# Optimization experiments

Measured on AMD Instinct MI355X. Metric: run time of the kernel, lower is better.

## Reference

```python
import jax, jax.numpy as jnp
import numpy as np

BETA = 1.0
EPS = 1e-12  # F.normalize eps

def _normalize(x):
    # F.normalize(x, dim=1): x shape (B, N, 1)
    n = jnp.sqrt(jnp.sum(x * x, axis=1, keepdims=True))
    return x / jnp.maximum(n, EPS)

def _step(M, x):
    return _normalize(jnp.matmul(M, x))

def _eigval(M, x):
    # x^T M x / ||x||^2, x: (B, N, 1)
    Mx = jnp.matmul(M, x)                          # (B, N, 1)
    num = jnp.sum(Mx * x, axis=(1, 2))             # (B,)
    den = jnp.sum(x * x, axis=(1, 2))              # (B,)
    return num / den

def setup_inputs() -> dict:
    key = jax.random.key(0)
    kA, kx = jax.random.split(key)
    A = jax.random.normal(kA, (64, 512, 28, 28), dtype=jnp.float32)
    x0 = jax.random.normal(kx, (64, 512, 1), dtype=jnp.float32)
    return {"A": A, "x0": x0}

def reference(A, x0):
    B, C, H, W = A.shape
    Wm = A.reshape(B, C, H * W)                    # (B, C, HW)
    AAT = jnp.einsum('bcd,bed->bce', Wm, Wm)       # (B, C, C)

    # --- dominant_eigenvalue(AAT): first call initializes last_x (no grad, 3 iters) ---
    xi = _normalize(x0)
    for _ in range(3):
        xi = _step(AAT, xi)
    xi = jax.lax.stop_gradient(xi)                 # last_x after no-grad init
    x1 = _step(AAT, xi)                            # 1 differentiable iter
    largest = _eigval(AAT, x1)                     # (B,)
    last_x = jax.lax.stop_gradient(x1)             # self.last_x = x.detach()

    # --- dominant_eigenvalue(AAT - largest*I): reuses last_x, 1 iter ---
    I = jnp.eye(C, dtype=A.dtype)[None]            # (1, C, C)
    A2 = AAT - largest[:, None, None] * I
    x2 = _step(A2, last_x)
    tmp = _eigval(A2, x2)

    smallest = tmp + largest
    penalty = BETA * (largest / smallest - 1.0) ** 2
    return jnp.sum(penalty) / B
```

## Files before the change

### kernel.cpp

```cpp
#include <hip/hip_runtime.h>
#include <math.h>


#define BB 64
#define CC 512
#define DD 784
#define DCH 16
#define NSPLIT 7
#define NCHPS 7
#define F4PR 196
#define BF4 100352
#define FEPS 1e-12f

__device__ __forceinline__ void gload16(const float4* gp, float4* lp) {
    __builtin_amdgcn_global_load_lds(
        (const __attribute__((address_space(1))) void*)gp,
        (__attribute__((address_space(3))) void*)lp, 16, 0, 0);
}

__device__ __forceinline__ float blk_reduce(float s, float* red) {
    for (int off = 32; off; off >>= 1) s += __shfl_down(s, off, 64);
    int w = threadIdx.x >> 6;
    if ((threadIdx.x & 63) == 0) red[w] = s;
    __syncthreads();
    float t = red[0] + red[1] + red[2] + red[3];
    __syncthreads();
    return t;
}

__global__ __launch_bounds__(256, 3)
void k_repack(const float* __restrict__ A, float* __restrict__ T) {
    __shared__ float4 lds4[16 * F4PR];
    const int tid = threadIdx.x, lane = tid & 63, w = tid >> 6;
    const int b = blockIdx.y, c0 = blockIdx.x * 16;
    const float4* src4 = (const float4*)A + ((size_t)b * CC + c0) * F4PR;
#pragma unroll
    for (int i = 0; i < 12; i++)
        gload16(src4 + i * 256 + w * 64 + lane, lds4 + i * 256 + w * 64);
    if (w == 0) gload16(src4 + 3072 + lane, lds4 + 3072);
    __syncthreads();
    float4* dst4 = (float4*)T + (size_t)b * BF4;
#pragma unroll
    for (int j = 0; j < 13; j++) {
        int idx = j * 256 + tid;
        if (idx < 3136) {
            int chq = idx >> 4, i = idx & 15;
            dst4[(size_t)chq * CC + c0 + i] = lds4[i * F4PR + chq];
        }
    }
}

template <bool RP>
__global__ __launch_bounds__(256, 2)
void k_step(const float* __restrict__ M, const float* __restrict__ xin,
            const int nparts, float* __restrict__ vout) {
    __shared__ float xs[CC];
    __shared__ float vws[4][CC];
    __shared__ float red[4];

    const int tid = threadIdx.x;
    const int b = blockIdx.y, s = blockIdx.x;
    const int lane = tid & 63, w = tid >> 6;
    const float4* Mb = (const float4*)M + (size_t)b * BF4;

    const float* xp = xin + (size_t)b * nparts * CC;
    float xv0 = 0.f, xv1 = 0.f;
    for (int p = 0; p < nparts; p++) {
        xv0 += xp[p * CC + tid];
        xv1 += xp[p * CC + tid + 256];
    }
    float ss = blk_reduce(xv0 * xv0 + xv1 * xv1, red);
    float rn = 1.0f / fmaxf(sqrtf(ss), FEPS);
    xs[tid] = xv0 * rn;
    xs[tid + 256] = xv1 * rn;
    __syncthreads();

    float xk[8];
#pragma unroll
    for (int k = 0; k < 8; k++) xk[k] = xs[lane + 64 * k];

    const int ch0 = s * NCHPS;
    float4 a[2][8];
    float vk[8] = {0.f, 0.f, 0.f, 0.f, 0.f, 0.f, 0.f, 0.f};

    auto load = [&](int ch, float4* dst) {
        if (RP) {
            const float4* g = Mb + (size_t)(ch * 4 + w) * CC + lane;
#pragma unroll
            for (int k = 0; k < 8; k++) dst[k] = g[64 * k];
        } else {
            const float4* g = Mb + (size_t)lane * F4PR + ch * 4 + w;
#pragma unroll
            for (int k = 0; k < 8; k++) dst[k] = g[(size_t)64 * k * F4PR];
        }
    };

    load(ch0, a[0]);
#pragma unroll
    for (int j = 0; j < NCHPS; j++) {
        const int cb = j & 1;
        if (j + 1 < NCHPS) load(ch0 + j + 1, a[cb ^ 1]);

        float4 ua = make_float4(0.f, 0.f, 0.f, 0.f);
#pragma unroll
        for (int k = 0; k < 8; k++) {
            ua.x += a[cb][k].x * xk[k]; ua.y += a[cb][k].y * xk[k];
            ua.z += a[cb][k].z * xk[k]; ua.w += a[cb][k].w * xk[k];
        }
#pragma unroll
        for (int off = 1; off < 64; off <<= 1) {
            ua.x += __shfl_xor(ua.x, off, 64);
            ua.y += __shfl_xor(ua.y, off, 64);
            ua.z += __shfl_xor(ua.z, off, 64);
            ua.w += __shfl_xor(ua.w, off, 64);
        }

#pragma unroll
        for (int k = 0; k < 8; k++)
            vk[k] += a[cb][k].x * ua.x + a[cb][k].y * ua.y +
                     a[cb][k].z * ua.z + a[cb][k].w * ua.w;
    }

#pragma unroll
    for (int k = 0; k < 8; k++) vws[w][lane + 64 * k] = vk[k];
    __syncthreads();
    float* vp = vout + ((size_t)b * NSPLIT + s) * CC;
    vp[tid]       = vws[0][tid] + vws[1][tid] + vws[2][tid] + vws[3][tid];
    vp[tid + 256] = vws[0][tid + 256] + vws[1][tid + 256] +
                    vws[2][tid + 256] + vws[3][tid + 256];
}

__global__ void k_mid(const float* __restrict__ t4, const float* __restrict__ t5,
                      float* __restrict__ acc, float* __restrict__ y) {
    __shared__ float red[4];
    int b = blockIdx.x;
    const float* p4 = t4 + (size_t)b * NSPLIT * CC;
    const float* p5 = t5 + (size_t)b * NSPLIT * CC;
    float a0 = 0.f, a1 = 0.f, b0 = 0.f, b1 = 0.f;
    for (int p = 0; p < NSPLIT; p++) {
        a0 += p4[p * CC + threadIdx.x]; a1 += p4[p * CC + threadIdx.x + 256];
        b0 += p5[p * CC + threadIdx.x]; b1 += p5[p * CC + threadIdx.x + 256];
    }
    float ss4 = blk_reduce(a0 * a0 + a1 * a1, red);
    float rn = 1.0f / fmaxf(sqrtf(ss4), FEPS);
    float x10 = a0 * rn, x11 = a1 * rn;
    float num = blk_reduce(b0 * x10 + b1 * x11, red);
    float den = blk_reduce(x10 * x10 + x11 * x11, red);
    float largest = num / den;
    float* yp = y + (size_t)b * CC;
    yp[threadIdx.x] = b0 - largest * x10;
    yp[threadIdx.x + 256] = b1 - largest * x11;
    if (threadIdx.x == 0) acc[b * 8 + 0] = largest;
}

__global__ void k_fin2(const float* __restrict__ w, const float* __restrict__ y,
                       float* __restrict__ acc) {
    __shared__ float red[4];
    int b = blockIdx.x;
    const float* wp = w + (size_t)b * NSPLIT * CC;
    const float* yp = y + (size_t)b * CC;
    float w0 = 0.f, w1 = 0.f;
    for (int p = 0; p < NSPLIT; p++) {
        w0 += wp[p * CC + threadIdx.x];
        w1 += wp[p * CC + threadIdx.x + 256];
    }
    float y0 = yp[threadIdx.x], y1 = yp[threadIdx.x + 256];
    float ssy = blk_reduce(y0 * y0 + y1 * y1, red);
    float rn = 1.0f / fmaxf(sqrtf(ssy), FEPS);
    float x20 = y0 * rn, x21 = y1 * rn;
    float dotwx = blk_reduce(w0 * x20 + w1 * x21, red);
    float den2 = blk_reduce(x20 * x20 + x21 * x21, red);
    if (threadIdx.x == 0) { acc[b * 8 + 1] = dotwx; acc[b * 8 + 2] = den2; }
}

__global__ void k_out(const float* __restrict__ acc, float* __restrict__ out) {
    int b = threadIdx.x;
    float largest = acc[b * 8 + 0];
    float dotwx   = acc[b * 8 + 1];
    float den2    = acc[b * 8 + 2];
    float tmp = (dotwx - largest * den2) / den2;
    float smallest = tmp + largest;
    float r = largest / smallest - 1.0f;
    float pen = r * r;
    for (int off = 32; off; off >>= 1) pen += __shfl_down(pen, off, 64);
    if (b == 0) out[0] = pen / (float)BB;
}

extern "C" void kernel_launch(void* const* d_in, const int* in_sizes, int n_in,
                              void* d_out, int out_size, void* d_ws, size_t ws_size,
                              hipStream_t stream) {
    const float* A  = (const float*)d_in[0];
    const float* x0 = (const float*)d_in[1];
    float* out = (float*)d_out;
    float* ws = (float*)d_ws;

    float* acc = ws;
    float* y   = ws + 512;
    float* PA  = y + BB * CC;
    float* PB  = PA + BB * NSPLIT * CC;
    float* T   = PB + BB * NSPLIT * CC;
    const size_t need = ((size_t)492032 + (size_t)BB * BF4 * 4) * sizeof(float);

    dim3 gS(NSPLIT, BB);
    if (ws_size >= need) {
        k_repack<<<dim3(32, BB), 256, 0, stream>>>(A, T);
        k_step<true><<<gS, 256, 0, stream>>>(T, x0, 1, PA);
        k_step<true><<<gS, 256, 0, stream>>>(T, PA, NSPLIT, PB);
        k_step<true><<<gS, 256, 0, stream>>>(T, PB, NSPLIT, PA);
        k_step<true><<<gS, 256, 0, stream>>>(T, PA, NSPLIT, PB);
        k_step<true><<<gS, 256, 0, stream>>>(T, PB, NSPLIT, PA);
        k_mid<<<BB, 256, 0, stream>>>(PB, PA, acc, y);
        k_step<true><<<gS, 256, 0, stream>>>(T, y, 1, PB);
        k_fin2<<<BB, 256, 0, stream>>>(PB, y, acc);
    } else {
        k_step<false><<<gS, 256, 0, stream>>>(A, x0, 1, PA);
        k_step<false><<<gS, 256, 0, stream>>>(A, PA, NSPLIT, PB);
        k_step<false><<<gS, 256, 0, stream>>>(A, PB, NSPLIT, PA);
        k_step<false><<<gS, 256, 0, stream>>>(A, PA, NSPLIT, PB);
        k_step<false><<<gS, 256, 0, stream>>>(A, PB, NSPLIT, PA);
        k_mid<<<BB, 256, 0, stream>>>(PB, PA, acc, y);
        k_step<false><<<gS, 256, 0, stream>>>(A, y, 1, PB);
        k_fin2<<<BB, 256, 0, stream>>>(PB, y, acc);
    }
    k_out<<<1, 64, 0, stream>>>(acc, out);
}
```

Baseline: 274.2 us.

## Split matvec into one chunk per block and hoist normalization into separate kernel

The step kernel now gives each block a single 4-float4 chunk of the d dimension (49 splits instead of 7 with double-buffered loops). Input normalization moves out of every step block into a small per-batch k_norm kernel, so blocks no longer each redo the partial-sum reduction. The repack kernel uses 8-row tiles with higher occupancy. This raises parallelism and occupancy but adds several extra kernel launches and larger partial buffers (49 partials per batch) to reduce.

```diff
diff --git a/kernel.cpp b/kernel.cpp
--- a/kernel.cpp
+++ b/kernel.cpp
@@ -5,9 +5,8 @@
 #define BB 64
 #define CC 512
 #define DD 784
-#define DCH 16
-#define NSPLIT 7
-#define NCHPS 7
+#define NCH 49
+#define QTOT 196
 #define F4PR 196
 #define BF4 100352
 #define FEPS 1e-12f
@@ -28,142 +27,140 @@
     return t;
 }
 
-__global__ __launch_bounds__(256, 3)
+__global__ __launch_bounds__(256, 6)
 void k_repack(const float* __restrict__ A, float* __restrict__ T) {
-    __shared__ float4 lds4[16 * F4PR];
+    __shared__ float4 lds4[8 * F4PR];
     const int tid = threadIdx.x, lane = tid & 63, w = tid >> 6;
-    const int b = blockIdx.y, c0 = blockIdx.x * 16;
-    const float4* src4 = (const float4*)A + ((size_t)b * CC + c0) * F4PR;
-#pragma unroll
-    for (int i = 0; i < 12; i++)
+    const int b = blockIdx.y, R0 = blockIdx.x * 8;
+    const float4* src4 = (const float4*)A + ((size_t)b * CC + R0) * F4PR;
+#pragma unroll
+    for (int i = 0; i < 6; i++)
         gload16(src4 + i * 256 + w * 64 + lane, lds4 + i * 256 + w * 64);
-    if (w == 0) gload16(src4 + 3072 + lane, lds4 + 3072);
+    if (w == 0 && lane < 32) gload16(src4 + 1536 + lane, lds4 + 1536);
     __syncthreads();
     float4* dst4 = (float4*)T + (size_t)b * BF4;
 #pragma unroll
-    for (int j = 0; j < 13; j++) {
+    for (int j = 0; j < 7; j++) {
         int idx = j * 256 + tid;
-        if (idx < 3136) {
-            int chq = idx >> 4, i = idx & 15;
-            dst4[(size_t)chq * CC + c0 + i] = lds4[i * F4PR + chq];
+        if (idx < 8 * F4PR) {
+            int chq = idx >> 3, i = idx & 7;
+            dst4[(size_t)chq * CC + R0 + i] = lds4[i * F4PR + chq];
         }
     }
 }
 
+__global__ void k_norm(const float* __restrict__ in, const int nparts,
+                       float* __restrict__ out) {
+    __shared__ float red[4];
+    int b = blockIdx.x;
+    const float* ip = in + (size_t)b * nparts * CC;
+    float v0 = 0.f, v1 = 0.f;
+    for (int p = 0; p < nparts; p++) {
+        v0 += ip[p * CC + threadIdx.x];
+        v1 += ip[p * CC + threadIdx.x + 256];
+    }
+    float ss = blk_reduce(v0 * v0 + v1 * v1, red);
+    float rn = 1.0f / fmaxf(sqrtf(ss), FEPS);
+    float* op = out + (size_t)b * CC;
+    op[threadIdx.x] = v0 * rn;
+    op[threadIdx.x + 256] = v1 * rn;
+}
+
 template <bool RP>
-__global__ __launch_bounds__(256, 2)
-void k_step(const float* __restrict__ M, const float* __restrict__ xin,
-            const int nparts, float* __restrict__ vout) {
+__global__ __launch_bounds__(256, 4)
+void k_step(const float* __restrict__ M, const float* __restrict__ xhat,
+            float* __restrict__ vout) {
     __shared__ float xs[CC];
     __shared__ float vws[4][CC];
-    __shared__ float red[4];
 
     const int tid = threadIdx.x;
     const int b = blockIdx.y, s = blockIdx.x;
     const int lane = tid & 63, w = tid >> 6;
+    const int chq = s * 4 + w;
     const float4* Mb = (const float4*)M + (size_t)b * BF4;
 
-    const float* xp = xin + (size_t)b * nparts * CC;
-    float xv0 = 0.f, xv1 = 0.f;
-    for (int p = 0; p < nparts; p++) {
-        xv0 += xp[p * CC + tid];
-        xv1 += xp[p * CC + tid + 256];
-    }
-    float ss = blk_reduce(xv0 * xv0 + xv1 * xv1, red);
-    float rn = 1.0f / fmaxf(sqrtf(ss), FEPS);
-    xs[tid] = xv0 * rn;
-    xs[tid + 256] = xv1 * rn;
-    __syncthreads();
-
+    float4 a[8];
+    if (RP) {
+        const float4* g = Mb + (size_t)chq * CC + lane;
+#pragma unroll
+        for (int k = 0; k < 8; k++) a[k] = g[64 * k];
+    } else {
+        const float4* g = Mb + (size_t)lane * F4PR + chq;
+#pragma unroll
+        for (int k = 0; k < 8; k++) a[k] = g[(size_t)64 * k * F4PR];
+    }
+
+    const float* xp = xhat + (size_t)b * CC;
+    xs[tid] = xp[tid];
+    xs[tid + 256] = xp[tid + 256];
+    __syncthreads();
     float xk[8];
 #pragma unroll
     for (int k = 0; k < 8; k++) xk[k] = xs[lane + 64 * k];
 
-    const int ch0 = s * NCHPS;
-    float4 a[2][8];
-    float vk[8] = {0.f, 0.f, 0.f, 0.f, 0.f, 0.f, 0.f, 0.f};
-
-    auto load = [&](int ch, float4* dst) {
-        if (RP) {
-            const float4* g = Mb + (size_t)(ch * 4 + w) * CC + lane;
-#pragma unroll
-            for (int k = 0; k < 8; k++) dst[k] = g[64 * k];
-        } else {
-            const float4* g = Mb + (size_t)lane * F4PR + ch * 4 + w;
-#pragma unroll
-            for (int k = 0; k < 8; k++) dst[k] = g[(size_t)64 * k * F4PR];
-        }
-    };
-
-    load(ch0, a[0]);
-#pragma unroll
-    for (int j = 0; j < NCHPS; j++) {
-        const int cb = j & 1;
-        if (j + 1 < NCHPS) load(ch0 + j + 1, a[cb ^ 1]);
-
-        float4 ua = make_float4(0.f, 0.f, 0.f, 0.f);
-#pragma unroll
-        for (int k = 0; k < 8; k++) {
-            ua.x += a[cb][k].x * xk[k]; ua.y += a[cb][k].y * xk[k];
-            ua.z += a[cb][k].z * xk[k]; ua.w += a[cb][k].w * xk[k];
-        }
-#pragma unroll
-        for (int off = 1; off < 64; off <<= 1) {
-            ua.x += __shfl_xor(ua.x, off, 64);
-            ua.y += __shfl_xor(ua.y, off, 64);
-            ua.z += __shfl_xor(ua.z, off, 64);
-            ua.w += __shfl_xor(ua.w, off, 64);
-        }
-
-#pragma unroll
-        for (int k = 0; k < 8; k++)
-            vk[k] += a[cb][k].x * ua.x + a[cb][k].y * ua.y +
-                     a[cb][k].z * ua.z + a[cb][k].w * ua.w;
-    }
+    float4 ua = make_float4(0.f, 0.f, 0.f, 0.f);
+#pragma unroll
+    for (int k = 0; k < 8; k++) {
+        ua.x += a[k].x * xk[k]; ua.y += a[k].y * xk[k];
+        ua.z += a[k].z * xk[k]; ua.w += a[k].w * xk[k];
+    }
+#pragma unroll
+    for (int off = 1; off < 64; off <<= 1) {
+        ua.x += __shfl_xor(ua.x, off, 64);
+        ua.y += __shfl_xor(ua.y, off, 64);
+        ua.z += __shfl_xor(ua.z, off, 64);
+        ua.w += __shfl_xor(ua.w, off, 64);
+    }
+
+    float vk[8];
+#pragma unroll
+    for (int k = 0; k < 8; k++)
+        vk[k] = a[k].x * ua.x + a[k].y * ua.y + a[k].z * ua.z + a[k].w * ua.w;
 
 #pragma unroll
     for (int k = 0; k < 8; k++) vws[w][lane + 64 * k] = vk[k];
     __syncthreads();
-    float* vp = vout + ((size_t)b * NSPLIT + s) * CC;
+    float* vp = vout + ((size_t)b * NCH + s) * CC;
     vp[tid]       = vws[0][tid] + vws[1][tid] + vws[2][tid] + vws[3][tid];
     vp[tid + 256] = vws[0][tid + 256] + vws[1][tid + 256] +
                     vws[2][tid + 256] + vws[3][tid + 256];
 }
 
-__global__ void k_mid(const float* __restrict__ t4, const float* __restrict__ t5,
-                      float* __restrict__ acc, float* __restrict__ y) {
+__global__ void k_mid(const float* __restrict__ x1, const float* __restrict__ P,
+                      float* __restrict__ acc, float* __restrict__ yhat) {
     __shared__ float red[4];
     int b = blockIdx.x;
-    const float* p4 = t4 + (size_t)b * NSPLIT * CC;
-    const float* p5 = t5 + (size_t)b * NSPLIT * CC;
-    float a0 = 0.f, a1 = 0.f, b0 = 0.f, b1 = 0.f;
-    for (int p = 0; p < NSPLIT; p++) {
-        a0 += p4[p * CC + threadIdx.x]; a1 += p4[p * CC + threadIdx.x + 256];
-        b0 += p5[p * CC + threadIdx.x]; b1 += p5[p * CC + threadIdx.x + 256];
-    }
-    float ss4 = blk_reduce(a0 * a0 + a1 * a1, red);
-    float rn = 1.0f / fmaxf(sqrtf(ss4), FEPS);
-    float x10 = a0 * rn, x11 = a1 * rn;
-    float num = blk_reduce(b0 * x10 + b1 * x11, red);
+    const float* pp = P + (size_t)b * NCH * CC;
+    float m0 = 0.f, m1 = 0.f;
+    for (int p = 0; p < NCH; p++) {
+        m0 += pp[p * CC + threadIdx.x];
+        m1 += pp[p * CC + threadIdx.x + 256];
+    }
+    const float* xp = x1 + (size_t)b * CC;
+    float x10 = xp[threadIdx.x], x11 = xp[threadIdx.x + 256];
+    float num = blk_reduce(m0 * x10 + m1 * x11, red);
     float den = blk_reduce(x10 * x10 + x11 * x11, red);
     float largest = num / den;
-    float* yp = y + (size_t)b * CC;
-    yp[threadIdx.x] = b0 - largest * x10;
-    yp[threadIdx.x + 256] = b1 - largest * x11;
+    float y0 = m0 - largest * x10, y1 = m1 - largest * x11;
+    float ssy = blk_reduce(y0 * y0 + y1 * y1, red);
+    float rn = 1.0f / fmaxf(sqrtf(ssy), FEPS);
+    float* yp = yhat + (size_t)b * CC;
+    yp[threadIdx.x] = y0 * rn;
+    yp[threadIdx.x + 256] = y1 * rn;
     if (threadIdx.x == 0) acc[b * 8 + 0] = largest;
 }
 
-__global__ void k_fin2(const float* __restrict__ w, const float* __restrict__ y,
+__global__ void k_fin2(const float* __restrict__ P, const float* __restrict__ yhat,
                        float* __restrict__ acc) {
     __shared__ float red[4];
     int b = blockIdx.x;
-    const float* wp = w + (size_t)b * NSPLIT * CC;
-    const float* yp = y + (size_t)b * CC;
+    const float* pp = P + (size_t)b * NCH * CC;
     float w0 = 0.f, w1 = 0.f;
-    for (int p = 0; p < NSPLIT; p++) {
-        w0 += wp[p * CC + threadIdx.x];
-        w1 += wp[p * CC + threadIdx.x + 256];
-    }
+    for (int p = 0; p < NCH; p++) {
+        w0 += pp[p * CC + threadIdx.x];
+        w1 += pp[p * CC + threadIdx.x + 256];
+    }
+    const float* yp = yhat + (size_t)b * CC;
     float y0 = yp[threadIdx.x], y1 = yp[threadIdx.x + 256];
     float ssy = blk_reduce(y0 * y0 + y1 * y1, red);
     float rn = 1.0f / fmaxf(sqrtf(ssy), FEPS);
@@ -195,32 +192,44 @@
     float* ws = (float*)d_ws;
 
     float* acc = ws;
-    float* y   = ws + 512;
-    float* PA  = y + BB * CC;
-    float* PB  = PA + BB * NSPLIT * CC;
-    float* T   = PB + BB * NSPLIT * CC;
-    const size_t need = ((size_t)492032 + (size_t)BB * BF4 * 4) * sizeof(float);
-
-    dim3 gS(NSPLIT, BB);
+    float* X   = ws + 512;
+    float* Y   = X + BB * CC;
+    float* P   = Y + BB * CC;
+    float* T   = P + (size_t)BB * NCH * CC;
+    const size_t need =
+        ((size_t)512 + 2 * BB * CC + (size_t)BB * NCH * CC +
+         (size_t)BB * CC * DD) * sizeof(float);
+
+    dim3 gS(NCH, BB);
     if (ws_size >= need) {
-        k_repack<<<dim3(32, BB), 256, 0, stream>>>(A, T);
-        k_step<true><<<gS, 256, 0, stream>>>(T, x0, 1, PA);
-        k_step<true><<<gS, 256, 0, stream>>>(T, PA, NSPLIT, PB);
-        k_step<true><<<gS, 256, 0, stream>>>(T, PB, NSPLIT, PA);
-        k_step<true><<<gS, 256, 0, stream>>>(T, PA, NSPLIT, PB);
-        k_step<true><<<gS, 256, 0, stream>>>(T, PB, NSPLIT, PA);
-        k_mid<<<BB, 256, 0, stream>>>(PB, PA, acc, y);
-        k_step<true><<<gS, 256, 0, stream>>>(T, y, 1, PB);
-        k_fin2<<<BB, 256, 0, stream>>>(PB, y, acc);
+        k_repack<<<dim3(CC / 8, BB), 256, 0, stream>>>(A, T);
+        k_norm<<<BB, 256, 0, stream>>>(x0, 1, X);
+        k_step<true><<<gS, 256, 0, stream>>>(T, X, P);
+        k_norm<<<BB, 256, 0, stream>>>(P, NCH, X);
+        k_step<true><<<gS, 256, 0, stream>>>(T, X, P);
+        k_norm<<<BB, 256, 0, stream>>>(P, NCH, X);
+        k_step<true><<<gS, 256, 0, stream>>>(T, X, P);
+        k_norm<<<BB, 256, 0, stream>>>(P, NCH, X);
+        k_step<true><<<gS, 256, 0, stream>>>(T, X, P);
+        k_norm<<<BB, 256, 0, stream>>>(P, NCH, X);
+        k_step<true><<<gS, 256, 0, stream>>>(T, X, P);
+        k_mid<<<BB, 256, 0, stream>>>(X, P, acc, Y);
+        k_step<true><<<gS, 256, 0, stream>>>(T, Y, P);
+        k_fin2<<<BB, 256, 0, stream>>>(P, Y, acc);
     } else {
-        k_step<false><<<gS, 256, 0, stream>>>(A, x0, 1, PA);
-        k_step<false><<<gS, 256, 0, stream>>>(A, PA, NSPLIT, PB);
-        k_step<false><<<gS, 256, 0, stream>>>(A, PB, NSPLIT, PA);
-        k_step<false><<<gS, 256, 0, stream>>>(A, PA, NSPLIT, PB);
-        k_step<false><<<gS, 256, 0, stream>>>(A, PB, NSPLIT, PA);
-        k_mid<<<BB, 256, 0, stream>>>(PB, PA, acc, y);
-        k_step<false><<<gS, 256, 0, stream>>>(A, y, 1, PB);
-        k_fin2<<<BB, 256, 0, stream>>>(PB, y, acc);
+        k_norm<<<BB, 256, 0, stream>>>(x0, 1, X);
+        k_step<false><<<gS, 256, 0, stream>>>(A, X, P);
+        k_norm<<<BB, 256, 0, stream>>>(P, NCH, X);
+        k_step<false><<<gS, 256, 0, stream>>>(A, X, P);
+        k_norm<<<BB, 256, 0, stream>>>(P, NCH, X);
+        k_step<false><<<gS, 256, 0, stream>>>(A, X, P);
+        k_norm<<<BB, 256, 0, stream>>>(P, NCH, X);
+        k_step<false><<<gS, 256, 0, stream>>>(A, X, P);
+        k_norm<<<BB, 256, 0, stream>>>(P, NCH, X);
+        k_step<false><<<gS, 256, 0, stream>>>(A, X, P);
+        k_mid<<<BB, 256, 0, stream>>>(X, P, acc, Y);
+        k_step<false><<<gS, 256, 0, stream>>>(A, Y, P);
+        k_fin2<<<BB, 256, 0, stream>>>(P, Y, acc);
     }
     k_out<<<1, 64, 0, stream>>>(acc, out);
 }
```

Result: slower. 332.0 us (+21.1%).

## Retile repack layout into 64-row blocks and split step kernel 16-way with prefetch

Applied to the files above, without the earlier changes.

The repacked matrix layout changes to 64-channel row blocks, so each wave's float4 loads cover a contiguous 1KB segment. Repack now uses XOR-swizzled LDS transposes over 64x28 tiles instead of global_load_lds. The step kernel splits work into 16 parts with interleaved quads and more blocks per CU. It issues the first two matrix loads before the x-normalisation reduction to hide latency. The cost is more partial sums for downstream kernels to reduce and uneven work, since some waves get 3 quads and others 4.

```diff
diff --git a/kernel.cpp b/kernel.cpp
--- a/kernel.cpp
+++ b/kernel.cpp
@@ -5,18 +5,13 @@
 #define BB 64
 #define CC 512
 #define DD 784
-#define DCH 16
-#define NSPLIT 7
-#define NCHPS 7
+#define NSPLIT 16
+#define NQ 196
 #define F4PR 196
 #define BF4 100352
+#define QT 28
+#define CBS 12544
 #define FEPS 1e-12f
-
-__device__ __forceinline__ void gload16(const float4* gp, float4* lp) {
-    __builtin_amdgcn_global_load_lds(
-        (const __attribute__((address_space(1))) void*)gp,
-        (__attribute__((address_space(3))) void*)lp, 16, 0, 0);
-}
 
 __device__ __forceinline__ float blk_reduce(float s, float* red) {
     for (int off = 32; off; off >>= 1) s += __shfl_down(s, off, 64);
@@ -28,30 +23,36 @@
     return t;
 }
 
-__global__ __launch_bounds__(256, 3)
+__global__ __launch_bounds__(256, 5)
 void k_repack(const float* __restrict__ A, float* __restrict__ T) {
-    __shared__ float4 lds4[16 * F4PR];
-    const int tid = threadIdx.x, lane = tid & 63, w = tid >> 6;
-    const int b = blockIdx.y, c0 = blockIdx.x * 16;
-    const float4* src4 = (const float4*)A + ((size_t)b * CC + c0) * F4PR;
-#pragma unroll
-    for (int i = 0; i < 12; i++)
-        gload16(src4 + i * 256 + w * 64 + lane, lds4 + i * 256 + w * 64);
-    if (w == 0) gload16(src4 + 3072 + lane, lds4 + 3072);
-    __syncthreads();
-    float4* dst4 = (float4*)T + (size_t)b * BF4;
-#pragma unroll
-    for (int j = 0; j < 13; j++) {
+    __shared__ float4 lds4[64 * QT];
+    const int tid = threadIdx.x;
+    const int b = blockIdx.y, tile = blockIdx.x;
+    const int cb = tile / 7, qt = tile % 7;
+    const int R0 = cb * 64, q0 = qt * QT;
+    const int r = tid >> 2, qg = tid & 3;
+    const float4* src = (const float4*)A +
+        ((size_t)b * CC + R0 + r) * F4PR + q0 + qg * 7;
+    float4 a[7];
+#pragma unroll
+    for (int j = 0; j < 7; j++) a[j] = src[j];
+    const int xr = (r >> 2) & 3;
+#pragma unroll
+    for (int j = 0; j < 7; j++)
+        lds4[r * QT + ((qg * 7 + j) ^ xr)] = a[j];
+    __syncthreads();
+    float4* dst = (float4*)T + (size_t)b * BF4 + (size_t)cb * CBS +
+                  (size_t)q0 * 64;
+#pragma unroll
+    for (int j = 0; j < 7; j++) {
         int idx = j * 256 + tid;
-        if (idx < 3136) {
-            int chq = idx >> 4, i = idx & 15;
-            dst4[(size_t)chq * CC + c0 + i] = lds4[i * F4PR + chq];
-        }
+        int chq = idx >> 6, i = idx & 63;
+        dst[idx] = lds4[i * QT + (chq ^ ((i >> 2) & 3))];
     }
 }
 
 template <bool RP>
-__global__ __launch_bounds__(256, 2)
+__global__ __launch_bounds__(256, 4)
 void k_step(const float* __restrict__ M, const float* __restrict__ xin,
             const int nparts, float* __restrict__ vout) {
     __shared__ float xs[CC];
@@ -61,51 +62,29 @@
     const int tid = threadIdx.x;
     const int b = blockIdx.y, s = blockIdx.x;
     const int lane = tid & 63, w = tid >> 6;
+    const int q0 = s * 4 + w;
     const float4* Mb = (const float4*)M + (size_t)b * BF4;
 
-    const float* xp = xin + (size_t)b * nparts * CC;
-    float xv0 = 0.f, xv1 = 0.f;
-    for (int p = 0; p < nparts; p++) {
-        xv0 += xp[p * CC + tid];
-        xv1 += xp[p * CC + tid + 256];
-    }
-    float ss = blk_reduce(xv0 * xv0 + xv1 * xv1, red);
-    float rn = 1.0f / fmaxf(sqrtf(ss), FEPS);
-    xs[tid] = xv0 * rn;
-    xs[tid + 256] = xv1 * rn;
-    __syncthreads();
-
     float xk[8];
-#pragma unroll
-    for (int k = 0; k < 8; k++) xk[k] = xs[lane + 64 * k];
-
-    const int ch0 = s * NCHPS;
-    float4 a[2][8];
     float vk[8] = {0.f, 0.f, 0.f, 0.f, 0.f, 0.f, 0.f, 0.f};
 
-    auto load = [&](int ch, float4* dst) {
+    auto loadq = [&](int q, float4* d) {
         if (RP) {
-            const float4* g = Mb + (size_t)(ch * 4 + w) * CC + lane;
-#pragma unroll
-            for (int k = 0; k < 8; k++) dst[k] = g[64 * k];
+            const float4* g = Mb + (size_t)q * 64 + lane;
+#pragma unroll
+            for (int k = 0; k < 8; k++) d[k] = g[(size_t)k * CBS];
         } else {
-            const float4* g = Mb + (size_t)lane * F4PR + ch * 4 + w;
-#pragma unroll
-            for (int k = 0; k < 8; k++) dst[k] = g[(size_t)64 * k * F4PR];
+            const float4* g = Mb + (size_t)lane * F4PR + q;
+#pragma unroll
+            for (int k = 0; k < 8; k++) d[k] = g[(size_t)64 * k * F4PR];
         }
     };
-
-    load(ch0, a[0]);
-#pragma unroll
-    for (int j = 0; j < NCHPS; j++) {
-        const int cb = j & 1;
-        if (j + 1 < NCHPS) load(ch0 + j + 1, a[cb ^ 1]);
-
+    auto computeq = [&](const float4* a) {
         float4 ua = make_float4(0.f, 0.f, 0.f, 0.f);
 #pragma unroll
         for (int k = 0; k < 8; k++) {
-            ua.x += a[cb][k].x * xk[k]; ua.y += a[cb][k].y * xk[k];
-            ua.z += a[cb][k].z * xk[k]; ua.w += a[cb][k].w * xk[k];
+            ua.x += a[k].x * xk[k]; ua.y += a[k].y * xk[k];
+            ua.z += a[k].z * xk[k]; ua.w += a[k].w * xk[k];
         }
 #pragma unroll
         for (int off = 1; off < 64; off <<= 1) {
@@ -114,12 +93,37 @@
             ua.z += __shfl_xor(ua.z, off, 64);
             ua.w += __shfl_xor(ua.w, off, 64);
         }
-
 #pragma unroll
         for (int k = 0; k < 8; k++)
-            vk[k] += a[cb][k].x * ua.x + a[cb][k].y * ua.y +
-                     a[cb][k].z * ua.z + a[cb][k].w * ua.w;
-    }
+            vk[k] += a[k].x * ua.x + a[k].y * ua.y +
+                     a[k].z * ua.z + a[k].w * ua.w;
+    };
+
+    float4 ra[8], rb[8];
+    loadq(q0, ra);
+    loadq(q0 + 64, rb);
+
+    const float* xp = xin + (size_t)b * nparts * CC;
+    float xv0 = 0.f, xv1 = 0.f;
+    for (int p = 0; p < nparts; p++) {
+        xv0 += xp[p * CC + tid];
+        xv1 += xp[p * CC + tid + 256];
+    }
+    float ss = blk_reduce(xv0 * xv0 + xv1 * xv1, red);
+    float rn = 1.0f / fmaxf(sqrtf(ss), FEPS);
+    xs[tid] = xv0 * rn;
+    xs[tid + 256] = xv1 * rn;
+    __syncthreads();
+#pragma unroll
+    for (int k = 0; k < 8; k++) xk[k] = xs[lane + 64 * k];
+
+    computeq(ra);
+    loadq(q0 + 128, ra);
+    computeq(rb);
+    const bool has4 = (q0 + 192) < NQ;
+    if (has4) loadq(q0 + 192, rb);
+    computeq(ra);
+    if (has4) computeq(rb);
 
 #pragma unroll
     for (int k = 0; k < 8; k++) vws[w][lane + 64 * k] = vk[k];
@@ -195,32 +199,34 @@
     float* ws = (float*)d_ws;
 
     float* acc = ws;
-    float* y   = ws + 512;
-    float* PA  = y + BB * CC;
-    float* PB  = PA + BB * NSPLIT * CC;
-    float* T   = PB + BB * NSPLIT * CC;
-    const size_t need = ((size_t)492032 + (size_t)BB * BF4 * 4) * sizeof(float);
+    float* Y   = ws + 512;
+    float* PA  = Y + BB * CC;
+    float* PB  = PA + (size_t)BB * NSPLIT * CC;
+    float* T   = PB + (size_t)BB * NSPLIT * CC;
+    const size_t need =
+        ((size_t)512 + BB * CC + 2 * (size_t)BB * NSPLIT * CC +
+         (size_t)BB * CC * DD) * sizeof(float);
 
     dim3 gS(NSPLIT, BB);
     if (ws_size >= need) {
-        k_repack<<<dim3(32, BB), 256, 0, stream>>>(A, T);
+        k_repack<<<dim3(56, BB), 256, 0, stream>>>(A, T);
         k_step<true><<<gS, 256, 0, stream>>>(T, x0, 1, PA);
         k_step<true><<<gS, 256, 0, stream>>>(T, PA, NSPLIT, PB);
         k_step<true><<<gS, 256, 0, stream>>>(T, PB, NSPLIT, PA);
         k_step<true><<<gS, 256, 0, stream>>>(T, PA, NSPLIT, PB);
         k_step<true><<<gS, 256, 0, stream>>>(T, PB, NSPLIT, PA);
-        k_mid<<<BB, 256, 0, stream>>>(PB, PA, acc, y);
-        k_step<true><<<gS, 256, 0, stream>>>(T, y, 1, PB);
-        k_fin2<<<BB, 256, 0, stream>>>(PB, y, acc);
+        k_mid<<<BB, 256, 0, stream>>>(PB, PA, acc, Y);
+        k_step<true><<<gS, 256, 0, stream>>>(T, Y, 1, PB);
+        k_fin2<<<BB, 256, 0, stream>>>(PB, Y, acc);
     } else {
         k_step<false><<<gS, 256, 0, stream>>>(A, x0, 1, PA);
         k_step<false><<<gS, 256, 0, stream>>>(A, PA, NSPLIT, PB);
         k_step<false><<<gS, 256, 0, stream>>>(A, PB, NSPLIT, PA);
         k_step<false><<<gS, 256, 0, stream>>>(A, PA, NSPLIT, PB);
         k_step<false><<<gS, 256, 0, stream>>>(A, PB, NSPLIT, PA);
-        k_mid<<<BB, 256, 0, stream>>>(PB, PA, acc, y);
-        k_step<false><<<gS, 256, 0, stream>>>(A, y, 1, PB);
-        k_fin2<<<BB, 256, 0, stream>>>(PB, y, acc);
+        k_mid<<<BB, 256, 0, stream>>>(PB, PA, acc, Y);
+        k_step<false><<<gS, 256, 0, stream>>>(A, Y, 1, PB);
+        k_fin2<<<BB, 256, 0, stream>>>(PB, Y, acc);
     }
     k_out<<<1, 64, 0, stream>>>(acc, out);
 }
```

Result: slower. 446.4 us (+62.8%).
